# Optimization experiments

Measured on AMD Instinct MI355X. Metric: run time of the kernel, lower is better.

## Reference

```python
import jax, jax.numpy as jnp
import numpy as np

L, B, E, H, NH = 128, 32, 128, 256, 8
NUM_NODE, ETA = 20000, 100


def setup_inputs() -> dict:
    key = jax.random.key(0)
    ks = jax.random.split(key, 24)
    s = 0.05
    rn = lambda k, sh: jax.random.normal(k, sh, dtype=jnp.float32) * s
    return {
        "node": jax.random.randint(ks[0], (L, B), 0, NUM_NODE + 1),
        "ts": jax.random.normal(ks[1], (L, B, 2), dtype=jnp.float32),
        "seq_lengths": jnp.sort(jax.random.randint(ks[2], (B,), 64, L + 1))[::-1],
        "embed_table": rn(ks[3], (NUM_NODE + 1, E)),
        "Wih0": rn(ks[4], (3 * H, E + 2)), "Whh0": rn(ks[5], (3 * H, H)),
        "bih0": rn(ks[6], (3 * H,)), "bhh0": rn(ks[7], (3 * H,)),
        "Wih1": rn(ks[8], (3 * H, H)), "Whh1": rn(ks[9], (3 * H, H)),
        "bih1": rn(ks[10], (3 * H,)), "bhh1": rn(ks[11], (3 * H,)),
        "Wa0": rn(ks[12], (E, 2 * E)), "ba0": rn(ks[13], (E,)),
        "Wa1": rn(ks[14], (NH, E)), "ba1": rn(ks[15], (NH,)),
        "Wf0": rn(ks[16], (168, H * (NH + 1))), "bf0": rn(ks[17], (168,)),
        "Wf1": rn(ks[18], (ETA, 168)), "bf1": rn(ks[19], (ETA,)),
    }


def gru_layer(x, Wih, Whh, bih, bhh, lengths):
    # x: [L, B, in]; PyTorch GRU cell, with pack/pad semantics:
    # hidden frozen and output zeroed for t >= length (emulates pack_padded_sequence).
    Lx, Bx, _ = x.shape

    def step(h, xs):
        x_t, t = xs
        gi = x_t @ Wih.T + bih          # [B, 3H]
        gh = h @ Whh.T + bhh            # [B, 3H]
        ir, iz, in_ = jnp.split(gi, 3, axis=-1)
        hr, hz, hn = jnp.split(gh, 3, axis=-1)
        r = jax.nn.sigmoid(ir + hr)
        z = jax.nn.sigmoid(iz + hz)
        n = jnp.tanh(in_ + r * hn)
        h_new = (1.0 - z) * n + z * h
        valid = (t < lengths)[:, None]
        h = jnp.where(valid, h_new, h)
        return h, jnp.where(valid, h_new, jnp.zeros_like(h_new))

    h0 = jnp.zeros((Bx, Whh.shape[1]), x.dtype)
    hT, outs = jax.lax.scan(step, h0, (x, jnp.arange(Lx)))
    return outs, hT


def reference(node, ts, seq_lengths, embed_table,
              Wih0, Whh0, bih0, bhh0, Wih1, Whh1, bih1, bhh1,
              Wa0, ba0, Wa1, ba1, Wf0, bf0, Wf1, bf1):
    e = embed_table[node]                          # [L, B, E]
    embeds = jnp.concatenate([e, ts], axis=-1)     # [L, B, E+2]

    # pairwise attention: a[i,j] = e[j], b[i,j] = e[i] (repeat + transpose)
    a = jnp.broadcast_to(e[None], (L, L, B, E))
    b = jnp.broadcast_to(e[:, None], (L, L, B, E))
    pair = jnp.concatenate([a, b], axis=-1)        # [L, L, B, 2E]
    hid = jax.nn.relu(pair @ Wa0.T + ba0)          # [L, L, B, E]
    w = (hid @ Wa1.T + ba1).sum(axis=1)            # [L, B, NH]

    # multiplicative length mask, then softmax over time axis (as in original)
    mask = (jnp.arange(L)[:, None] < seq_lengths[None, :]).astype(w.dtype)[..., None]
    w = jax.nn.softmax(w * mask, axis=0)           # [L, B, NH]

    out0, _ = gru_layer(embeds, Wih0, Whh0, bih0, bhh0, seq_lengths)
    out1, hT = gru_layer(out0, Wih1, Whh1, bih1, bhh1, seq_lengths)  # [L,B,H], [B,H]

    ctx = jnp.einsum('lbh,lbd->bhd', w, out1).reshape(B, NH * H)     # [B, NH*H]
    z = jnp.concatenate([ctx, hT], axis=-1) @ Wf0.T + bf0
    z = jax.nn.selu(z)
    logits = z @ Wf1.T + bf1
    return jax.nn.log_softmax(logits, axis=-1)
```

## Files before the change

kernel.cpp:

```cpp
#include <hip/hip_runtime.h>
#include <hip/hip_bf16.h>

#define LL 128
#define BB 32
#define EE 128
#define HH 256
#define NHH 8
#define G3 768
#define IN0 130
#define ETA 100
#define F1 168
#define CLSIN 2304

typedef _Float16 half_t;
typedef __attribute__((ext_vector_type(2))) _Float16 half2v;
typedef __attribute__((ext_vector_type(16))) unsigned int uint16v;

#if defined(__has_builtin)
#if __has_builtin(__builtin_amdgcn_fdot2)
#define HAVE_FDOT2 1
#endif
#endif

__device__ __forceinline__ float fdot2f(half2v a, half2v b, float c) {
#ifdef HAVE_FDOT2
  return __builtin_amdgcn_fdot2(a, b, c, false);
#else
  return c + (float)a.x * (float)b.x + (float)a.y * (float)b.y;
#endif
}
__device__ __forceinline__ float fdot2u(unsigned int a, unsigned int b, float c) {
  return fdot2f(__builtin_bit_cast(half2v, a), __builtin_bit_cast(half2v, b), c);
}

#define BARRIER_LDS() __asm__ volatile("s_waitcnt lgkmcnt(0)\n\ts_barrier" ::: "memory")

__device__ __forceinline__ float sigmoidf_(float x) { return 1.0f / (1.0f + __expf(-x)); }
__device__ __forceinline__ float tanhf_(float x) { return 1.0f - 2.0f / (__expf(2.0f * x) + 1.0f); }

__global__ void prep_kernel(
    const float* __restrict__ Wa0, const float* __restrict__ Wih0,
    const float* __restrict__ Wih1, const float* __restrict__ Whh0,
    const float* __restrict__ Whh1,
    half_t* __restrict__ Wa0Ta, half_t* __restrict__ Wa0Tb,
    half2v* __restrict__ Wih0T2, half2v* __restrict__ Wih1T2,
    half_t* __restrict__ Whh0h, half_t* __restrict__ Whh1h)
{
  int idx = blockIdx.x * blockDim.x + threadIdx.x;
  const int n1 = 16384, n2 = 16384, n3 = 65 * 768, n4 = 128 * 768, n5 = 196608;
  if (idx < n1) {
    int d = idx >> 7, k = idx & 127;
    Wa0Ta[idx] = (half_t)Wa0[k * 256 + d];
  } else if ((idx -= n1) < n2) {
    int d = idx >> 7, k = idx & 127;
    Wa0Tb[idx] = (half_t)Wa0[k * 256 + 128 + d];
  } else if ((idx -= n2) < n3) {
    int d2 = idx / 768, r = idx % 768;
    half2v w; w.x = (half_t)Wih0[r * IN0 + 2 * d2]; w.y = (half_t)Wih0[r * IN0 + 2 * d2 + 1];
    Wih0T2[idx] = w;
  } else if ((idx -= n3) < n4) {
    int d2 = idx / 768, r = idx % 768;
    half2v w; w.x = (half_t)Wih1[r * HH + 2 * d2]; w.y = (half_t)Wih1[r * HH + 2 * d2 + 1];
    Wih1T2[idx] = w;
  } else if ((idx -= n4) < n5) {
    Whh0h[idx] = (half_t)Whh0[idx];
  } else if ((idx -= n5) < n5) {
    Whh1h[idx] = (half_t)Whh1[idx];
  }
}

__global__ void embed_uv_kernel(
    const int* __restrict__ node,
    const float* __restrict__ table,
    const half_t* __restrict__ Wa0Ta,
    const half_t* __restrict__ Wa0Tb,
    const float* __restrict__ ba0,
    half2v* __restrict__ e_h2,
    float* __restrict__ U,
    float* __restrict__ V)
{
  int lb = blockIdx.x;
  int k = threadIdx.x;
  __shared__ float es[EE];
  int n = node[lb];
  float ev = table[(size_t)n * EE + k];
  es[k] = ev;
  __syncthreads();
  if (k < 64) {
    half2v p; p.x = (half_t)es[2 * k]; p.y = (half_t)es[2 * k + 1];
    e_h2[(size_t)lb * 64 + k] = p;
  }
  float u = 0.f, v = ba0[k];
  #pragma unroll 8
  for (int d = 0; d < EE; ++d) {
    float x = es[d];
    u += (float)Wa0Ta[d * EE + k] * x;
    v += (float)Wa0Tb[d * EE + k] * x;
  }
  U[(size_t)lb * EE + k] = u;
  V[(size_t)lb * EE + k] = v;
}

__global__ __launch_bounds__(128) void attn_w_kernel(
    const float* __restrict__ U, const float* __restrict__ V,
    const float* __restrict__ Wa1,
    const float* __restrict__ ba1,
    float* __restrict__ wpre)
{
  int ig = blockIdx.x >> 5;
  int b = blockIdx.x & 31;
  int i0 = ig * 4;
  int k = threadIdx.x;
  float vk[4];
  #pragma unroll
  for (int ii = 0; ii < 4; ++ii) vk[ii] = V[((size_t)(i0 + ii) * BB + b) * EE + k];
  float wa[NHH], acc[4][NHH];
  #pragma unroll
  for (int h = 0; h < NHH; ++h) wa[h] = Wa1[h * EE + k];
  #pragma unroll
  for (int ii = 0; ii < 4; ++ii)
    #pragma unroll
    for (int h = 0; h < NHH; ++h) acc[ii][h] = 0.f;
  for (int j = 0; j < LL; ++j) {
    float u = U[((size_t)j * BB + b) * EE + k];
    #pragma unroll
    for (int ii = 0; ii < 4; ++ii) {
      float tv = fmaxf(u + vk[ii], 0.f);
      #pragma unroll
      for (int h = 0; h < NHH; ++h) acc[ii][h] += wa[h] * tv;
    }
  }
  __shared__ float part[2][32];
  int wave = k >> 6, lane = k & 63;
  #pragma unroll
  for (int ii = 0; ii < 4; ++ii)
    #pragma unroll
    for (int h = 0; h < NHH; ++h) {
      float a = acc[ii][h];
      #pragma unroll
      for (int off = 32; off > 0; off >>= 1) a += __shfl_xor(a, off, 64);
      if (lane == 0) part[wave][ii * 8 + h] = a;
    }
  __syncthreads();
  if (k < 32) {
    int ii = k >> 3, h = k & 7;
    float w = part[0][k] + part[1][k] + (float)LL * ba1[h];
    wpre[((size_t)(i0 + ii) * BB + b) * NHH + h] = w;
  }
}

__global__ void attn_softmax_kernel(
    const float* __restrict__ wpre, const int* __restrict__ slen,
    float* __restrict__ wsoft)
{
  int b = blockIdx.x >> 3;
  int h = blockIdx.x & 7;
  int l = threadIdx.x;
  int len = slen[b];
  float x = wpre[((size_t)l * BB + b) * NHH + h];
  float xv = (l < len) ? x : 0.f;
  float m = xv;
  #pragma unroll
  for (int off = 32; off > 0; off >>= 1) m = fmaxf(m, __shfl_xor(m, off, 64));
  __shared__ float sm[2], ss[2];
  int wave = l >> 6;
  if ((l & 63) == 0) sm[wave] = m;
  __syncthreads();
  m = fmaxf(sm[0], sm[1]);
  float e = __expf(xv - m);
  float s = e;
  #pragma unroll
  for (int off = 32; off > 0; off >>= 1) s += __shfl_xor(s, off, 64);
  if ((l & 63) == 0) ss[wave] = s;
  __syncthreads();
  s = ss[0] + ss[1];
  wsoft[((size_t)l * BB + b) * NHH + h] = e / s;
}

__global__ __launch_bounds__(256) void gi0_kernel(
    const half2v* __restrict__ e_h2, const float* __restrict__ ts,
    const half2v* __restrict__ W2,
    const float* __restrict__ bih,
    float* __restrict__ gi)
{
  int lb0 = blockIdx.x * 8;
  int tid = threadIdx.x;
  __shared__ half2v xs2[8][66];
  for (int idx = tid; idx < 512; idx += 256) {
    int q = idx >> 6, d2 = idx & 63;
    xs2[q][d2] = e_h2[(size_t)(lb0 + q) * 64 + d2];
  }
  if (tid < 8) {
    half2v t2; t2.x = (half_t)ts[(lb0 + tid) * 2]; t2.y = (half_t)ts[(lb0 + tid) * 2 + 1];
    xs2[tid][64] = t2;
  }
  __syncthreads();
  float acc[8][3];
  #pragma unroll
  for (int q = 0; q < 8; ++q) { acc[q][0] = 0.f; acc[q][1] = 0.f; acc[q][2] = 0.f; }
  for (int d2 = 0; d2 < 65; ++d2) {
    half2v w0 = W2[d2 * 768 + tid];
    half2v w1 = W2[d2 * 768 + 256 + tid];
    half2v w2 = W2[d2 * 768 + 512 + tid];
    #pragma unroll
    for (int q = 0; q < 8; ++q) {
      half2v x = xs2[q][d2];
      acc[q][0] = fdot2f(w0, x, acc[q][0]);
      acc[q][1] = fdot2f(w1, x, acc[q][1]);
      acc[q][2] = fdot2f(w2, x, acc[q][2]);
    }
  }
  float b0 = bih[tid], b1 = bih[256 + tid], b2 = bih[512 + tid];
  #pragma unroll
  for (int q = 0; q < 8; ++q) {
    float* gp = gi + (size_t)(lb0 + q) * G3;
    gp[tid] = acc[q][0] + b0; gp[256 + tid] = acc[q][1] + b1; gp[512 + tid] = acc[q][2] + b2;
  }
}

__global__ __launch_bounds__(256) void gi1_kernel(
    const float* __restrict__ out0,
    const half2v* __restrict__ W2,
    const float* __restrict__ bih,
    float* __restrict__ gi)
{
  int lb0 = blockIdx.x * 8;
  int tid = threadIdx.x;
  __shared__ half2v xs2[8][128];
  for (int idx = tid; idx < 1024; idx += 256) {
    int q = idx >> 7, d2 = idx & 127;
    float2 v = ((const float2*)(out0 + (size_t)(lb0 + q) * HH))[d2];
    half2v x; x.x = (half_t)v.x; x.y = (half_t)v.y;
    xs2[q][d2] = x;
  }
  __syncthreads();
  float acc[8][3];
  #pragma unroll
  for (int q = 0; q < 8; ++q) { acc[q][0] = 0.f; acc[q][1] = 0.f; acc[q][2] = 0.f; }
  for (int d2 = 0; d2 < 128; ++d2) {
    half2v w0 = W2[d2 * 768 + tid];
    half2v w1 = W2[d2 * 768 + 256 + tid];
    half2v w2 = W2[d2 * 768 + 512 + tid];
    #pragma unroll
    for (int q = 0; q < 8; ++q) {
      half2v x = xs2[q][d2];
      acc[q][0] = fdot2f(w0, x, acc[q][0]);
      acc[q][1] = fdot2f(w1, x, acc[q][1]);
      acc[q][2] = fdot2f(w2, x, acc[q][2]);
    }
  }
  float b0 = bih[tid], b1 = bih[256 + tid], b2 = bih[512 + tid];
  #pragma unroll
  for (int q = 0; q < 8; ++q) {
    float* gp = gi + (size_t)(lb0 + q) * G3;
    gp[tid] = acc[q][0] + b0; gp[256 + tid] = acc[q][1] + b1; gp[512 + tid] = acc[q][2] + b2;
  }
}

__global__ __launch_bounds__(512, 2) void gru_scan_kernel(
    const half_t* __restrict__ Whhh,
    const float* __restrict__ bhh,
    const float* __restrict__ gi,
    const int* __restrict__ slen,
    float* __restrict__ out,
    float* __restrict__ hT)
{
  const int b = blockIdx.x;
  const int tid = threadIdx.x;
  const int s = tid & 3;
  const int g = tid >> 2;
  __shared__ __align__(16) uint4 h4[4 * 9];
  __shared__ float p5[768 * 5];

  uint16v W[12];
  #pragma unroll
  for (int r = 0; r < 6; ++r) {
    const uint4* wp = (const uint4*)(Whhh + (size_t)(6 * g + r) * HH + 64 * s);
    #pragma unroll
    for (int j = 0; j < 8; ++j) {
      uint4 v = wp[j];
      int base = 4 * j;
      if (base < 16) {
        W[2 * r][base] = v.x; W[2 * r][base + 1] = v.y;
        W[2 * r][base + 2] = v.z; W[2 * r][base + 3] = v.w;
      } else {
        W[2 * r + 1][base - 16] = v.x; W[2 * r + 1][base - 15] = v.y;
        W[2 * r + 1][base - 14] = v.z; W[2 * r + 1][base - 13] = v.w;
      }
    }
  }

  const int len = slen[b];
  float bhr = 0.f, bhz = 0.f, bhn = 0.f, hold = 0.f;
  if (tid < HH) {
    bhr = bhh[tid]; bhz = bhh[HH + tid]; bhn = bhh[2 * HH + tid];
  }
  if (tid < 36) { uint4 z; z.x = z.y = z.z = z.w = 0u; h4[tid] = z; }
  __syncthreads();

  const float* gib = gi + (size_t)b * G3;
  float* outb = out + (size_t)b * HH;

  #pragma unroll 1
  for (int t = 0; t < LL; ++t) {
    __asm__ volatile(""
        : "+v"(W[0]), "+v"(W[1]), "+v"(W[2]), "+v"(W[3]), "+v"(W[4]),
          "+v"(W[5]), "+v"(W[6]), "+v"(W[7]), "+v"(W[8]), "+v"(W[9]),
          "+v"(W[10]), "+v"(W[11]));
    float g0 = 0.f, g1 = 0.f, g2 = 0.f;
    if (tid < HH) {
      const float* gp = gib + (size_t)t * (BB * G3);
      g0 = gp[tid]; g1 = gp[HH + tid]; g2 = gp[2 * HH + tid];
    }
    float acc[6] = {0.f, 0.f, 0.f, 0.f, 0.f, 0.f};
    #pragma unroll
    for (int c = 0; c < 4; ++c) {
      uint4 ha = h4[s * 9 + 2 * c];
      uint4 hb = h4[s * 9 + 2 * c + 1];
      unsigned int hu[8] = {ha.x, ha.y, ha.z, ha.w, hb.x, hb.y, hb.z, hb.w};
      #pragma unroll
      for (int r = 0; r < 6; ++r) {
        #pragma unroll
        for (int i = 0; i < 8; ++i) {
          int idx = 8 * c + i;
          unsigned int wv = (idx < 16) ? W[2 * r][idx] : W[2 * r + 1][idx - 16];
          acc[r] = fdot2u(wv, hu[i], acc[r]);
        }
      }
    }
    #pragma unroll
    for (int r = 0; r < 6; ++r)
      p5[(6 * g + r) * 5 + s] = acc[r];
    BARRIER_LDS();
    if (tid < HH) {
      int b0 = tid * 5, b1 = (HH + tid) * 5, b2 = (2 * HH + tid) * 5;
      float srz = (p5[b0] + p5[b0 + 1]) + (p5[b0 + 2] + p5[b0 + 3]);
      float sz  = (p5[b1] + p5[b1 + 1]) + (p5[b1 + 2] + p5[b1 + 3]);
      float sn  = (p5[b2] + p5[b2 + 1]) + (p5[b2 + 2] + p5[b2 + 3]);
      float r_ = sigmoidf_(g0 + srz + bhr);
      float z_ = sigmoidf_(g1 + sz + bhz);
      float n_ = tanhf_(g2 + r_ * (sn + bhn));
      float hnew = (1.f - z_) * n_ + z_ * hold;
      bool valid = t < len;
      hold = valid ? hnew : hold;
      ((half_t*)(h4 + (tid >> 6) * 9))[tid & 63] = (half_t)hold;
      outb[(size_t)t * (BB * HH) + tid] = valid ? hnew : 0.f;
    }
    BARRIER_LDS();
  }
  if (tid < HH) hT[(size_t)b * HH + tid] = hold;
}

__global__ void ctx_kernel(
    const float* __restrict__ wsoft, const float* __restrict__ out1,
    float* __restrict__ ctx)
{
  int b = blockIdx.x >> 3, h = blockIdx.x & 7;
  int d = threadIdx.x;
  float acc = 0.f;
  for (int l = 0; l < LL; ++l) {
    float w = wsoft[((size_t)l * BB + b) * NHH + h];
    acc += w * out1[((size_t)l * BB + b) * HH + d];
  }
  ctx[(size_t)b * (NHH * HH) + h * HH + d] = acc;
}

__global__ __launch_bounds__(512) void final_kernel(
    const float* __restrict__ ctx, const float* __restrict__ hT,
    const float* __restrict__ Wf0,
    const float* __restrict__ bf0,
    const float* __restrict__ Wf1,
    const float* __restrict__ bf1,
    float* __restrict__ outp)
{
  int b = blockIdx.x;
  int tid = threadIdx.x;
  int wave = tid >> 6, lane = tid & 63;
  __shared__ float4 xs4[CLSIN / 4];
  __shared__ float zs[F1];
  __shared__ float ls[ETA];
  float* xs = (float*)xs4;
  for (int i = tid; i < NHH * HH; i += 512) xs[i] = ctx[(size_t)b * (NHH * HH) + i];
  if (tid < HH) xs[NHH * HH + tid] = hT[(size_t)b * HH + tid];
  __syncthreads();
  for (int r = wave; r < F1; r += 8) {
    const float4* wp = (const float4*)(Wf0 + (size_t)r * CLSIN);
    float acc = 0.f;
    #pragma unroll
    for (int i = 0; i < CLSIN / 4 / 64; ++i) {
      float4 w = wp[lane + 64 * i];
      float4 x = xs4[lane + 64 * i];
      acc += w.x * x.x + w.y * x.y + w.z * x.z + w.w * x.w;
    }
    #pragma unroll
    for (int off = 32; off > 0; off >>= 1) acc += __shfl_xor(acc, off, 64);
    if (lane == 0) {
      float x = acc + bf0[r];
      const float alpha = 1.6732632423543772f, scale = 1.0507009873554805f;
      zs[r] = scale * (x > 0.f ? x : alpha * (__expf(x) - 1.f));
    }
  }
  __syncthreads();
  for (int r = wave; r < ETA; r += 8) {
    float acc = 0.f;
    for (int k = lane; k < F1; k += 64) acc += Wf1[r * F1 + k] * zs[k];
    #pragma unroll
    for (int off = 32; off > 0; off >>= 1) acc += __shfl_xor(acc, off, 64);
    if (lane == 0) ls[r] = acc + bf1[r];
  }
  __syncthreads();
  if (wave == 0) {
    float v0 = (lane < ETA) ? ls[lane] : -1e30f;
    float v1 = (lane + 64 < ETA) ? ls[lane + 64] : -1e30f;
    float m = fmaxf(v0, v1);
    #pragma unroll
    for (int off = 32; off > 0; off >>= 1) m = fmaxf(m, __shfl_xor(m, off, 64));
    float s = __expf(v0 - m) + __expf(v1 - m);
    #pragma unroll
    for (int off = 32; off > 0; off >>= 1) s += __shfl_xor(s, off, 64);
    float lse = m + __logf(s);
    if (lane < ETA) outp[(size_t)b * ETA + lane] = v0 - lse;
    if (lane + 64 < ETA) outp[(size_t)b * ETA + lane + 64] = v1 - lse;
  }
}

extern "C" void kernel_launch(void* const* d_in, const int* in_sizes, int n_in,
                              void* d_out, int out_size, void* d_ws, size_t ws_size,
                              hipStream_t stream) {
  const int*   node  = (const int*)d_in[0];
  const float* ts    = (const float*)d_in[1];
  const int*   slen  = (const int*)d_in[2];
  const float* table = (const float*)d_in[3];
  const float* Wih0  = (const float*)d_in[4];
  const float* Whh0  = (const float*)d_in[5];
  const float* bih0  = (const float*)d_in[6];
  const float* bhh0  = (const float*)d_in[7];
  const float* Wih1  = (const float*)d_in[8];
  const float* Whh1  = (const float*)d_in[9];
  const float* bih1  = (const float*)d_in[10];
  const float* bhh1  = (const float*)d_in[11];
  const float* Wa0   = (const float*)d_in[12];
  const float* ba0   = (const float*)d_in[13];
  const float* Wa1   = (const float*)d_in[14];
  const float* ba1   = (const float*)d_in[15];
  const float* Wf0   = (const float*)d_in[16];
  const float* bf0   = (const float*)d_in[17];
  const float* Wf1   = (const float*)d_in[18];
  const float* bf1   = (const float*)d_in[19];

  char* ws = (char*)d_ws;
  size_t off = 0;
  auto alloc = [&](size_t n) { void* p = (void*)(ws + off); off += (n + 255) & ~(size_t)255; return p; };

  half2v* e_h2 = (half2v*)alloc((size_t)LL * BB * 64 * 4);
  float* U     = (float*)alloc((size_t)LL * BB * EE * 4);
  float* V     = (float*)alloc((size_t)LL * BB * EE * 4);
  float* gi    = (float*)alloc((size_t)LL * BB * G3 * 4);
  float* out0  = (float*)alloc((size_t)LL * BB * HH * 4);
  float* out1  = (float*)alloc((size_t)LL * BB * HH * 4);
  float* hTb   = (float*)alloc((size_t)BB * HH * 4);
  float* wpre  = (float*)alloc((size_t)LL * BB * NHH * 4);
  float* wsoft = (float*)alloc((size_t)LL * BB * NHH * 4);
  float* ctxb  = (float*)alloc((size_t)BB * NHH * HH * 4);
  half_t* Wa0Ta = (half_t*)alloc((size_t)128 * 128 * 2);
  half_t* Wa0Tb = (half_t*)alloc((size_t)128 * 128 * 2);
  half2v* Wih0T2 = (half2v*)alloc((size_t)65 * 768 * 4);
  half2v* Wih1T2 = (half2v*)alloc((size_t)128 * 768 * 4);
  half_t* Whh0h = (half_t*)alloc((size_t)G3 * HH * 2);
  half_t* Whh1h = (half_t*)alloc((size_t)G3 * HH * 2);
  if (off > ws_size) return;

  const int prep_total = 16384 + 16384 + 65 * 768 + 128 * 768 + 196608 + 196608;
  prep_kernel<<<(prep_total + 255) / 256, 256, 0, stream>>>(
      Wa0, Wih0, Wih1, Whh0, Whh1, Wa0Ta, Wa0Tb, Wih0T2, Wih1T2, Whh0h, Whh1h);
  embed_uv_kernel<<<LL * BB, 128, 0, stream>>>(node, table, Wa0Ta, Wa0Tb, ba0, e_h2, U, V);
  attn_w_kernel<<<(LL / 4) * BB, 128, 0, stream>>>(U, V, Wa1, ba1, wpre);
  attn_softmax_kernel<<<BB * NHH, 128, 0, stream>>>(wpre, slen, wsoft);
  gi0_kernel<<<LL * BB / 8, 256, 0, stream>>>(e_h2, ts, Wih0T2, bih0, gi);
  gru_scan_kernel<<<BB, 512, 0, stream>>>(Whh0h, bhh0, gi, slen, out0, hTb);
  gi1_kernel<<<LL * BB / 8, 256, 0, stream>>>(out0, Wih1T2, bih1, gi);
  gru_scan_kernel<<<BB, 512, 0, stream>>>(Whh1h, bhh1, gi, slen, out1, hTb);
  ctx_kernel<<<BB * NHH, 256, 0, stream>>>(wsoft, out1, ctxb);
  final_kernel<<<BB, 512, 0, stream>>>(ctxb, hTb, Wf0, bf0, Wf1, bf1, (float*)d_out);
}
```

Baseline: 583.0 us.

## Reduce GRU partial sums with lane shuffles and double-buffer hidden state

Each group of four lanes now holds the weight rows for two hidden units across all three gates, so the four K-slice partial sums can be combined with xor shuffles inside the wavefront instead of through a shared-memory partial buffer. Because the hidden vector is double-buffered, each timestep needs only one barrier instead of two, and the gate math runs on half of the lanes rather than the first 256 threads. The time loop is also unrolled by four. The cost is extra shuffle instructions and some redundant gate arithmetic in lanes that do not write results.

Measured after the change: 617.7 us. 6.0% more time.

```diff
diff --git a/kernel.cpp b/kernel.cpp
--- a/kernel.cpp
+++ b/kernel.cpp
@@ -269,86 +269,95 @@
   const int tid = threadIdx.x;
   const int s = tid & 3;
   const int g = tid >> 2;
-  __shared__ __align__(16) uint4 h4[4 * 9];
-  __shared__ float p5[768 * 5];
+  __shared__ __align__(16) uint4 hbuf[2][4 * 9];
 
   uint16v W[12];
   #pragma unroll
-  for (int r = 0; r < 6; ++r) {
-    const uint4* wp = (const uint4*)(Whhh + (size_t)(6 * g + r) * HH + 64 * s);
+  for (int rr = 0; rr < 6; ++rr) {
+    int row = ((rr >> 1) << 8) + 2 * g + (rr & 1);
+    const uint4* wp = (const uint4*)(Whhh + (size_t)row * HH + 64 * s);
     #pragma unroll
     for (int j = 0; j < 8; ++j) {
       uint4 v = wp[j];
       int base = 4 * j;
       if (base < 16) {
-        W[2 * r][base] = v.x; W[2 * r][base + 1] = v.y;
-        W[2 * r][base + 2] = v.z; W[2 * r][base + 3] = v.w;
+        W[2 * rr][base] = v.x; W[2 * rr][base + 1] = v.y;
+        W[2 * rr][base + 2] = v.z; W[2 * rr][base + 3] = v.w;
       } else {
-        W[2 * r + 1][base - 16] = v.x; W[2 * r + 1][base - 15] = v.y;
-        W[2 * r + 1][base - 14] = v.z; W[2 * r + 1][base - 13] = v.w;
+        W[2 * rr + 1][base - 16] = v.x; W[2 * rr + 1][base - 15] = v.y;
+        W[2 * rr + 1][base - 14] = v.z; W[2 * rr + 1][base - 13] = v.w;
       }
     }
   }
 
   const int len = slen[b];
+  const int u = 2 * g + (s & 1);
   float bhr = 0.f, bhz = 0.f, bhn = 0.f, hold = 0.f;
-  if (tid < HH) {
-    bhr = bhh[tid]; bhz = bhh[HH + tid]; bhn = bhh[2 * HH + tid];
-  }
-  if (tid < 36) { uint4 z; z.x = z.y = z.z = z.w = 0u; h4[tid] = z; }
+  if (s < 2) {
+    bhr = bhh[u]; bhz = bhh[HH + u]; bhn = bhh[2 * HH + u];
+  }
+  for (int i = tid; i < 72; i += 512) {
+    uint4 z; z.x = z.y = z.z = z.w = 0u; ((uint4*)hbuf)[i] = z;
+  }
   __syncthreads();
 
   const float* gib = gi + (size_t)b * G3;
   float* outb = out + (size_t)b * HH;
 
   #pragma unroll 1
-  for (int t = 0; t < LL; ++t) {
+  for (int t4 = 0; t4 < LL / 4; ++t4) {
     __asm__ volatile(""
         : "+v"(W[0]), "+v"(W[1]), "+v"(W[2]), "+v"(W[3]), "+v"(W[4]),
           "+v"(W[5]), "+v"(W[6]), "+v"(W[7]), "+v"(W[8]), "+v"(W[9]),
           "+v"(W[10]), "+v"(W[11]));
-    float g0 = 0.f, g1 = 0.f, g2 = 0.f;
-    if (tid < HH) {
-      const float* gp = gib + (size_t)t * (BB * G3);
-      g0 = gp[tid]; g1 = gp[HH + tid]; g2 = gp[2 * HH + tid];
-    }
-    float acc[6] = {0.f, 0.f, 0.f, 0.f, 0.f, 0.f};
-    #pragma unroll
-    for (int c = 0; c < 4; ++c) {
-      uint4 ha = h4[s * 9 + 2 * c];
-      uint4 hb = h4[s * 9 + 2 * c + 1];
-      unsigned int hu[8] = {ha.x, ha.y, ha.z, ha.w, hb.x, hb.y, hb.z, hb.w};
+    #pragma unroll
+    for (int tt = 0; tt < 4; ++tt) {
+      const int t = 4 * t4 + tt;
+      const uint4* rb = hbuf[t & 1];
+      uint4* wb = (uint4*)hbuf[(t & 1) ^ 1];
+      float g0 = 0.f, g1 = 0.f, g2 = 0.f;
+      if (s < 2) {
+        const float* gp = gib + (size_t)t * (BB * G3);
+        g0 = gp[u]; g1 = gp[HH + u]; g2 = gp[2 * HH + u];
+      }
+      float acc[6] = {0.f, 0.f, 0.f, 0.f, 0.f, 0.f};
       #pragma unroll
-      for (int r = 0; r < 6; ++r) {
+      for (int c = 0; c < 4; ++c) {
+        uint4 ha = rb[s * 9 + 2 * c];
+        uint4 hb = rb[s * 9 + 2 * c + 1];
+        unsigned int hu[8] = {ha.x, ha.y, ha.z, ha.w, hb.x, hb.y, hb.z, hb.w};
         #pragma unroll
-        for (int i = 0; i < 8; ++i) {
-          int idx = 8 * c + i;
-          unsigned int wv = (idx < 16) ? W[2 * r][idx] : W[2 * r + 1][idx - 16];
-          acc[r] = fdot2u(wv, hu[i], acc[r]);
+        for (int rr = 0; rr < 6; ++rr) {
+          #pragma unroll
+          for (int i = 0; i < 8; ++i) {
+            int idx = 8 * c + i;
+            unsigned int wv = (idx < 16) ? W[2 * rr][idx] : W[2 * rr + 1][idx - 16];
+            acc[rr] = fdot2u(wv, hu[i], acc[rr]);
+          }
         }
       }
-    }
-    #pragma unroll
-    for (int r = 0; r < 6; ++r)
-      p5[(6 * g + r) * 5 + s] = acc[r];
-    BARRIER_LDS();
-    if (tid < HH) {
-      int b0 = tid * 5, b1 = (HH + tid) * 5, b2 = (2 * HH + tid) * 5;
-      float srz = (p5[b0] + p5[b0 + 1]) + (p5[b0 + 2] + p5[b0 + 3]);
-      float sz  = (p5[b1] + p5[b1 + 1]) + (p5[b1 + 2] + p5[b1 + 3]);
-      float sn  = (p5[b2] + p5[b2 + 1]) + (p5[b2 + 2] + p5[b2 + 3]);
-      float r_ = sigmoidf_(g0 + srz + bhr);
-      float z_ = sigmoidf_(g1 + sz + bhz);
-      float n_ = tanhf_(g2 + r_ * (sn + bhn));
+      #pragma unroll
+      for (int rr = 0; rr < 6; ++rr) {
+        acc[rr] += __shfl_xor(acc[rr], 1, 64);
+        acc[rr] += __shfl_xor(acc[rr], 2, 64);
+      }
+      float rs = (s & 1) ? acc[1] : acc[0];
+      float zsum = (s & 1) ? acc[3] : acc[2];
+      float ns = (s & 1) ? acc[5] : acc[4];
+      float r_ = sigmoidf_(g0 + rs + bhr);
+      float z_ = sigmoidf_(g1 + zsum + bhz);
+      float n_ = tanhf_(g2 + r_ * (ns + bhn));
       float hnew = (1.f - z_) * n_ + z_ * hold;
       bool valid = t < len;
       hold = valid ? hnew : hold;
-      ((half_t*)(h4 + (tid >> 6) * 9))[tid & 63] = (half_t)hold;
-      outb[(size_t)t * (BB * HH) + tid] = valid ? hnew : 0.f;
-    }
-    BARRIER_LDS();
-  }
-  if (tid < HH) hT[(size_t)b * HH + tid] = hold;
+      if (s < 2) {
+        ((half_t*)(wb + (u >> 6) * 9))[u & 63] = (half_t)hold;
+        outb[(size_t)t * (BB * HH) + u] = valid ? hnew : 0.f;
+      }
+      BARRIER_LDS();
+    }
+  }
+  if (s < 2) hT[(size_t)b * HH + u] = hold;
 }
 
 __global__ void ctx_kernel(
```

## Use MFMA for GRU recurrent matvec and drop cross-thread partial-sum reduction

Applied to the files above, without the earlier changes.

The per-step h·Whh^T product in the GRU scan now runs on MFMA f16 16x16x32 instructions, with weights held as register A-fragments. The hidden vector is broadcast as the B operand, so every output column carries the same result and lanes with m==0 write directly to shared memory. This removes the long fdot2 chains and the four-way partial-sum reduction through shared memory. In exchange it spends 16x redundant MFMA work on the broadcast columns, and the 48 f16x8 weight fragments add register pressure.

Result: slower. 638.3 us (+9.5%).

```diff
diff --git a/kernel.cpp b/kernel.cpp
--- a/kernel.cpp
+++ b/kernel.cpp
@@ -14,7 +14,8 @@
 
 typedef _Float16 half_t;
 typedef __attribute__((ext_vector_type(2))) _Float16 half2v;
-typedef __attribute__((ext_vector_type(16))) unsigned int uint16v;
+typedef __attribute__((ext_vector_type(8))) _Float16 f16x8;
+typedef __attribute__((ext_vector_type(4))) float f32x4;
 
 #if defined(__has_builtin)
 #if __has_builtin(__builtin_amdgcn_fdot2)
@@ -28,9 +29,6 @@
 #else
   return c + (float)a.x * (float)b.x + (float)a.y * (float)b.y;
 #endif
-}
-__device__ __forceinline__ float fdot2u(unsigned int a, unsigned int b, float c) {
-  return fdot2f(__builtin_bit_cast(half2v, a), __builtin_bit_cast(half2v, b), c);
 }
 
 #define BARRIER_LDS() __asm__ volatile("s_waitcnt lgkmcnt(0)\n\ts_barrier" ::: "memory")
@@ -267,35 +265,30 @@
 {
   const int b = blockIdx.x;
   const int tid = threadIdx.x;
-  const int s = tid & 3;
-  const int g = tid >> 2;
-  __shared__ __align__(16) uint4 h4[4 * 9];
-  __shared__ float p5[768 * 5];
-
-  uint16v W[12];
-  #pragma unroll
-  for (int r = 0; r < 6; ++r) {
-    const uint4* wp = (const uint4*)(Whhh + (size_t)(6 * g + r) * HH + 64 * s);
-    #pragma unroll
-    for (int j = 0; j < 8; ++j) {
-      uint4 v = wp[j];
-      int base = 4 * j;
-      if (base < 16) {
-        W[2 * r][base] = v.x; W[2 * r][base + 1] = v.y;
-        W[2 * r][base + 2] = v.z; W[2 * r][base + 3] = v.w;
-      } else {
-        W[2 * r + 1][base - 16] = v.x; W[2 * r + 1][base - 15] = v.y;
-        W[2 * r + 1][base - 14] = v.z; W[2 * r + 1][base - 13] = v.w;
-      }
-    }
+  const int w = tid >> 6;
+  const int lane = tid & 63;
+  const int m = lane & 15;
+  const int kg = lane >> 4;
+
+  __shared__ __align__(16) half_t hshared[HH];
+  __shared__ __align__(16) float gsum[G3];
+
+  f16x8 A[48];
+  {
+    const half_t* wbase = Whhh + (size_t)(w * 96 + m) * HH + kg * 8;
+    #pragma unroll
+    for (int tl = 0; tl < 6; ++tl)
+      #pragma unroll
+      for (int kc = 0; kc < 8; ++kc)
+        A[tl * 8 + kc] = *(const f16x8*)(wbase + (size_t)(tl * 16) * HH + kc * 32);
   }
 
   const int len = slen[b];
   float bhr = 0.f, bhz = 0.f, bhn = 0.f, hold = 0.f;
   if (tid < HH) {
     bhr = bhh[tid]; bhz = bhh[HH + tid]; bhn = bhh[2 * HH + tid];
-  }
-  if (tid < 36) { uint4 z; z.x = z.y = z.z = z.w = 0u; h4[tid] = z; }
+    hshared[tid] = (half_t)0.f;
+  }
   __syncthreads();
 
   const float* gib = gi + (size_t)b * G3;
@@ -303,47 +296,35 @@
 
   #pragma unroll 1
   for (int t = 0; t < LL; ++t) {
-    __asm__ volatile(""
-        : "+v"(W[0]), "+v"(W[1]), "+v"(W[2]), "+v"(W[3]), "+v"(W[4]),
-          "+v"(W[5]), "+v"(W[6]), "+v"(W[7]), "+v"(W[8]), "+v"(W[9]),
-          "+v"(W[10]), "+v"(W[11]));
     float g0 = 0.f, g1 = 0.f, g2 = 0.f;
     if (tid < HH) {
       const float* gp = gib + (size_t)t * (BB * G3);
       g0 = gp[tid]; g1 = gp[HH + tid]; g2 = gp[2 * HH + tid];
     }
-    float acc[6] = {0.f, 0.f, 0.f, 0.f, 0.f, 0.f};
-    #pragma unroll
-    for (int c = 0; c < 4; ++c) {
-      uint4 ha = h4[s * 9 + 2 * c];
-      uint4 hb = h4[s * 9 + 2 * c + 1];
-      unsigned int hu[8] = {ha.x, ha.y, ha.z, ha.w, hb.x, hb.y, hb.z, hb.w};
+    f32x4 C[6];
+    #pragma unroll
+    for (int tl = 0; tl < 6; ++tl) C[tl] = (f32x4){0.f, 0.f, 0.f, 0.f};
+    #pragma unroll
+    for (int kc = 0; kc < 8; ++kc) {
+      f16x8 bf = *(const f16x8*)&hshared[kc * 32 + kg * 8];
       #pragma unroll
-      for (int r = 0; r < 6; ++r) {
-        #pragma unroll
-        for (int i = 0; i < 8; ++i) {
-          int idx = 8 * c + i;
-          unsigned int wv = (idx < 16) ? W[2 * r][idx] : W[2 * r + 1][idx - 16];
-          acc[r] = fdot2u(wv, hu[i], acc[r]);
-        }
-      }
-    }
-    #pragma unroll
-    for (int r = 0; r < 6; ++r)
-      p5[(6 * g + r) * 5 + s] = acc[r];
+      for (int tl = 0; tl < 6; ++tl)
+        C[tl] = __builtin_amdgcn_mfma_f32_16x16x32_f16(A[tl * 8 + kc], bf, C[tl], 0, 0, 0);
+    }
+    if (m == 0) {
+      #pragma unroll
+      for (int tl = 0; tl < 6; ++tl)
+        *(f32x4*)&gsum[w * 96 + tl * 16 + kg * 4] = C[tl];
+    }
     BARRIER_LDS();
     if (tid < HH) {
-      int b0 = tid * 5, b1 = (HH + tid) * 5, b2 = (2 * HH + tid) * 5;
-      float srz = (p5[b0] + p5[b0 + 1]) + (p5[b0 + 2] + p5[b0 + 3]);
-      float sz  = (p5[b1] + p5[b1 + 1]) + (p5[b1 + 2] + p5[b1 + 3]);
-      float sn  = (p5[b2] + p5[b2 + 1]) + (p5[b2 + 2] + p5[b2 + 3]);
-      float r_ = sigmoidf_(g0 + srz + bhr);
-      float z_ = sigmoidf_(g1 + sz + bhz);
-      float n_ = tanhf_(g2 + r_ * (sn + bhn));
+      float r_ = sigmoidf_(g0 + gsum[tid] + bhr);
+      float z_ = sigmoidf_(g1 + gsum[HH + tid] + bhz);
+      float n_ = tanhf_(g2 + r_ * (gsum[2 * HH + tid] + bhn));
       float hnew = (1.f - z_) * n_ + z_ * hold;
       bool valid = t < len;
       hold = valid ? hnew : hold;
-      ((half_t*)(h4 + (tid >> 6) * 9))[tid & 63] = (half_t)hold;
+      hshared[tid] = (half_t)hold;
       outb[(size_t)t * (BB * HH) + tid] = valid ? hnew : 0.f;
     }
     BARRIER_LDS();
```
